# Kernel tuning notes

Hardware: AMD Instinct MI355X
Metric: run time of the kernel (lower is better)

Reference implementation:

```python
import jax, jax.numpy as jnp
import numpy as np

B = 128        # graphs
NPG = 64       # nodes per graph (num_node)
N = B * NPG    # total nodes = 8192
IN = 16        # in_channels
D = 128        # d_model
OUT = 64       # out_channels
CAT = IN * NPG + NPG * NPG  # 5120
EPS = 1e-5


def _lin_init(k, fi, fo):
    s = 1.0 / np.sqrt(fi)
    kw, kb = jax.random.split(k)
    W = jax.random.uniform(kw, (fi, fo), jnp.float32, -s, s)
    b = jax.random.uniform(kb, (fo,), jnp.float32, -s, s)
    return W, b


def setup_inputs() -> dict:
    key = jax.random.key(0)
    ks = jax.random.split(key, 10)
    x = jax.random.normal(ks[0], (N, IN), jnp.float32)
    # complete graph (all i->j pairs, incl. self loops) per graph, offset per graph
    ii = np.repeat(np.arange(NPG), NPG)
    jj = np.tile(np.arange(NPG), NPG)
    off = (np.arange(B) * NPG)[:, None]
    row = (ii[None, :] + off).reshape(-1)
    col = (jj[None, :] + off).reshape(-1)
    edge_index = jnp.asarray(np.stack([row, col]), jnp.int32)  # [2, E]
    E = edge_index.shape[1]
    edge_weight = jax.random.uniform(ks[1], (E,), jnp.float32)
    batch = jnp.repeat(jnp.arange(B, dtype=jnp.int32), NPG)
    W1, b1 = _lin_init(ks[2], IN, D)
    W2, b2 = _lin_init(ks[3], D, D)
    Wm0, bm0 = _lin_init(ks[4], D + CAT, D)
    Wm1, bm1 = _lin_init(ks[5], D, D)
    Wm2, bm2 = _lin_init(ks[6], D, D)
    Wout, bout = _lin_init(ks[7], D, OUT)
    ones = jnp.ones((D,), jnp.float32)
    zeros = jnp.zeros((D,), jnp.float32)
    return dict(x=x, edge_index=edge_index, edge_weight=edge_weight, batch=batch,
                W1=W1, b1=b1, W2=W2, b2=b2,
                Wm0=Wm0, bm0=bm0, g0=ones, be0=zeros,
                Wm1=Wm1, bm1=bm1, g1=ones, be1=zeros,
                Wm2=Wm2, bm2=bm2, g2=ones, be2=zeros,
                Wout=Wout, bout=bout)


def _gcn_conv(h_in, row, col, ew, W, b):
    # PyG GCNConv: linear first, then D^-1/2 (A) D^-1/2 aggregation (self loops already present)
    h = h_in @ W                                             # [N, F]
    deg = jax.ops.segment_sum(ew, col, num_segments=N)       # in-degree by edge weight
    dinv = jnp.where(deg > 0, jax.lax.rsqrt(deg), 0.0)
    norm = dinv[row] * ew * dinv[col]                        # [E]
    out = jax.ops.segment_sum(norm[:, None] * h[row], col, num_segments=N)
    return out + b


def _bn(h, g, b):
    # BatchNorm1d, training-mode math (biased variance), eps=1e-5
    m = jnp.mean(h, axis=0)
    v = jnp.var(h, axis=0)
    return g * (h - m) * jax.lax.rsqrt(v + EPS) + b


def reference(x, edge_index, edge_weight, batch,
              W1, b1, W2, b2,
              Wm0, bm0, g0, be0,
              Wm1, bm1, g1, be1,
              Wm2, bm2, g2, be2,
              Wout, bout):
    row, col = edge_index[0], edge_index[1]
    h = _gcn_conv(x, row, col, edge_weight, W1, b1)
    h = jax.nn.relu(h)
    h = _gcn_conv(h, row, col, edge_weight, W2, b2)
    # global_mean_pool
    sums = jax.ops.segment_sum(h, batch, num_segments=B)
    cnt = jax.ops.segment_sum(jnp.ones((N,), h.dtype), batch, num_segments=B)
    pooled = sums / cnt[:, None]
    pooled = jax.nn.relu(pooled)
    feat = jnp.concatenate([pooled, x.reshape(B, -1), edge_weight.reshape(B, -1)], axis=1)
    feat = jax.nn.relu(feat)
    h = _bn(jax.nn.relu(feat @ Wm0 + bm0), g0, be0)
    h = _bn(jax.nn.relu(h @ Wm1 + bm1), g1, be1)
    h = _bn(jax.nn.relu(h @ Wm2 + bm2), g2, be2)
    return h @ Wout + bout
```

## Files before the change

### kernel.cpp

```cpp
#include <hip/hip_runtime.h>

#define NG 128
#define NPG 64
#define IN 16
#define DM 128
#define NOUT 64
#define EPG 4096
#define NGEMM 160
#define BN_EPS 1e-5f

__global__ __launch_bounds__(256) void k_front(
    const float* __restrict__ x, const float* __restrict__ ew,
    const float* __restrict__ W1, const float* __restrict__ b1,
    const float* __restrict__ Wm0,
    float* __restrict__ z, float* __restrict__ part, float* __restrict__ stats)
{
    __shared__ __align__(16) float u[15616];
    const int b = blockIdx.x, t = threadIdx.x;

    if (b < 128) {
        float* ew_s   = u;
        float* x_s    = u + 4096;
        float* W1_s   = u + 5120;
        float* P_s    = u + 7168;
        float* b1_s   = u + 15360;
        float* dinv_s = u + 15488;
        float* t_s    = u + 15552;
        float* zp     = u + 4096;
        const int g = b;
        if (b == 0) {
            for (int i = t; i < 768; i += 256) stats[i] = 0.f;
        }
        {
            const float4* ew4 = (const float4*)(ew + g * EPG);
            float4* ews4 = (float4*)ew_s;
            #pragma unroll
            for (int i = 0; i < 4; i++) ews4[t + 256 * i] = ew4[t + 256 * i];
            const int xi = t & 63, k4 = (t >> 6) * 4;
            float4 xv = *(const float4*)(x + g * NPG * IN + xi * IN + k4);
            x_s[(k4 + 0) * 64 + xi] = xv.x;
            x_s[(k4 + 1) * 64 + xi] = xv.y;
            x_s[(k4 + 2) * 64 + xi] = xv.z;
            x_s[(k4 + 3) * 64 + xi] = xv.w;
            ((float4*)W1_s)[t]       = ((const float4*)W1)[t];
            ((float4*)W1_s)[t + 256] = ((const float4*)W1)[t + 256];
            if (t < 128) b1_s[t] = b1[t];
        }
        __syncthreads();

        if (t < NPG) {
            float s = 0.f;
            #pragma unroll 8
            for (int i = 0; i < NPG; i++) s += ew_s[i * NPG + t];
            dinv_s[t] = (s > 0.f) ? rsqrtf(s) : 0.f;
        }
        __syncthreads();

        {
            const int j = t & 63, q = t >> 6;
            const float dj = dinv_s[j];
            for (int i = q * 16; i < q * 16 + 16; i++) {
                float vv = ew_s[i * NPG + j] * dj;
                #pragma unroll
                for (int off = 32; off > 0; off >>= 1) vv += __shfl_down(vv, off, 64);
                if (j == 0) t_s[i] = dinv_s[i] * vv * (1.f / 64.f);
            }
        }
        __syncthreads();

        {
            const int it = t & 15, ft = t >> 4;
            const int i0 = it * 4, f0 = ft * 8;
            float accp[4][8];
            #pragma unroll
            for (int a = 0; a < 4; a++)
                #pragma unroll
                for (int c = 0; c < 8; c++) accp[a][c] = 0.f;
            #pragma unroll
            for (int k = 0; k < IN; k++) {
                const float4 a4  = *(const float4*)(x_s + k * 64 + i0);
                const float4 b0v = *(const float4*)(W1_s + k * DM + f0);
                const float4 b1v = *(const float4*)(W1_s + k * DM + f0 + 4);
                const float av[4] = {a4.x, a4.y, a4.z, a4.w};
                const float bv[8] = {b0v.x, b0v.y, b0v.z, b0v.w, b1v.x, b1v.y, b1v.z, b1v.w};
                #pragma unroll
                for (int a = 0; a < 4; a++)
                    #pragma unroll
                    for (int c = 0; c < 8; c++) accp[a][c] += av[a] * bv[c];
            }
            #pragma unroll
            for (int a = 0; a < 4; a++) {
                float4* o = (float4*)(P_s + (i0 + a) * DM + f0);
                o[0] = make_float4(accp[a][0], accp[a][1], accp[a][2], accp[a][3]);
                o[1] = make_float4(accp[a][4], accp[a][5], accp[a][6], accp[a][7]);
            }
        }
        __syncthreads();

        for (int i = t; i < EPG; i += 256) ew_s[i] *= dinv_s[i >> 6];
        __syncthreads();

        {
            const int jt = t & 15, ft = t >> 4;
            const int j0 = jt * 4, f0 = ft * 8;
            float acc[4][8];
            #pragma unroll
            for (int a = 0; a < 4; a++)
                #pragma unroll
                for (int c = 0; c < 8; c++) acc[a][c] = 0.f;
            #pragma unroll 4
            for (int k = 0; k < 64; k++) {
                const float4 a4  = *(const float4*)(ew_s + k * 64 + j0);
                const float4 b0v = *(const float4*)(P_s + k * DM + f0);
                const float4 b1v = *(const float4*)(P_s + k * DM + f0 + 4);
                const float av[4] = {a4.x, a4.y, a4.z, a4.w};
                const float bv[8] = {b0v.x, b0v.y, b0v.z, b0v.w, b1v.x, b1v.y, b1v.z, b1v.w};
                #pragma unroll
                for (int a = 0; a < 4; a++)
                    #pragma unroll
                    for (int c = 0; c < 8; c++) acc[a][c] += av[a] * bv[c];
            }
            float zpart[8];
            #pragma unroll
            for (int c = 0; c < 8; c++) zpart[c] = 0.f;
            #pragma unroll
            for (int a = 0; a < 4; a++) {
                const float dj = dinv_s[j0 + a], tj = t_s[j0 + a];
                #pragma unroll
                for (int c = 0; c < 8; c++) {
                    float h = fmaxf(dj * acc[a][c] + b1_s[f0 + c], 0.f);
                    zpart[c] += tj * h;
                }
            }
            float4* zo = (float4*)(zp + jt * 132 + f0);
            zo[0] = make_float4(zpart[0], zpart[1], zpart[2], zpart[3]);
            zo[1] = make_float4(zpart[4], zpart[5], zpart[6], zpart[7]);
        }
        __syncthreads();

        if (t < 128) {
            float s = 0.f;
            #pragma unroll
            for (int jt = 0; jt < 16; jt++) s += zp[jt * 132 + t];
            z[g * DM + t] = s;
        }
    } else {
        const int c = b - 128;
        const int kc = c >> 1, fh = c & 1;
        float* a_s = u;
        float* b_s = u + 8448;

        const float* src; int stride, off;
        if (kc < 16) { src = x;  stride = 1024; off = kc * 64; }
        else         { src = ew; stride = 4096; off = (kc - 16) * 64; }
        const int K0 = 128 + kc * 64;

        #pragma unroll 4
        for (int it = 0; it < 32; it++) {
            int idx = it * 256 + t;
            int gg = idx >> 6, k = idx & 63;
            a_s[k * 132 + gg] = fmaxf(src[gg * stride + off + k], 0.f);
        }
        #pragma unroll 4
        for (int it = 0; it < 16; it++) {
            int idx = it * 256 + t;
            int k = idx >> 6, fl = idx & 63;
            b_s[k * 64 + fl] = Wm0[(K0 + k) * 128 + fh * 64 + fl];
        }
        __syncthreads();

        const int gthr = t & 31, fthr = t >> 5;
        const int g0 = gthr * 4, f0 = fthr * 8;
        float acc[4][8];
        #pragma unroll
        for (int i = 0; i < 4; i++)
            #pragma unroll
            for (int jx = 0; jx < 8; jx++) acc[i][jx] = 0.f;

        #pragma unroll 4
        for (int k = 0; k < 64; k++) {
            const float4 a4  = *(const float4*)(a_s + k * 132 + g0);
            const float4 c0v = *(const float4*)(b_s + k * 64 + f0);
            const float4 c1v = *(const float4*)(b_s + k * 64 + f0 + 4);
            const float av[4] = {a4.x, a4.y, a4.z, a4.w};
            const float bv[8] = {c0v.x, c0v.y, c0v.z, c0v.w, c1v.x, c1v.y, c1v.z, c1v.w};
            #pragma unroll
            for (int i = 0; i < 4; i++)
                #pragma unroll
                for (int jx = 0; jx < 8; jx++) acc[i][jx] += av[i] * bv[jx];
        }

        float* pp = part + c * 8192;
        #pragma unroll
        for (int i = 0; i < 4; i++) {
            float4* o = (float4*)(pp + (g0 + i) * 64 + f0);
            o[0] = make_float4(acc[i][0], acc[i][1], acc[i][2], acc[i][3]);
            o[1] = make_float4(acc[i][4], acc[i][5], acc[i][6], acc[i][7]);
        }
    }
}

__global__ __launch_bounds__(256) void k_reduce_bn0(
    const float* __restrict__ part, const float* __restrict__ zbuf,
    const float* __restrict__ W2, const float* __restrict__ b2,
    const float* __restrict__ Wm0, const float* __restrict__ bm0,
    float* __restrict__ v0, float* __restrict__ stats0)
{
    __shared__ __align__(16) float W2_s[16384];
    __shared__ __align__(16) float z_s[512];
    __shared__ float Wm0s[2048];
    __shared__ float pooled_s[4 * 130];
    __shared__ float pps[64];
    __shared__ float r1[256];
    __shared__ float sv[64], sv2[64];

    const int bx = blockIdx.x, t = threadIdx.x;
    const int fgrp = bx & 7, gt = bx >> 3;
    const int fsub = t & 15, gl = (t >> 4) & 3, ch = t >> 6;
    const int f = fgrp * 16 + fsub, g = gt * 4 + gl;
    const int fh = f >> 6, fl = f & 63;

    const float* p = part + (size_t)(2 * (ch * 20) + fh) * 8192 + g * 64 + fl;
    float v = 0.f;
    #pragma unroll 5
    for (int cc = 0; cc < 20; cc++) v += p[(size_t)cc * 2 * 8192];

    {
        const float4* w24 = (const float4*)W2;
        float4* w2s4 = (float4*)W2_s;
        #pragma unroll
        for (int i = 0; i < 16; i++) w2s4[t + 256 * i] = w24[t + 256 * i];
        if (t < 128) ((float4*)z_s)[t] = ((const float4*)(zbuf + gt * 512))[t];
        for (int idx = t; idx < 2048; idx += 256) {
            int k = idx >> 4, fs = idx & 15;
            Wm0s[idx] = Wm0[k * DM + fgrp * 16 + fs];
        }
    }
    r1[t] = v;
    __syncthreads();

    {
        const int gp = t >> 6, k0 = t & 63;
        float a0 = 0.f, a1 = 0.f;
        #pragma unroll 4
        for (int m = 0; m < DM; m++) {
            const float zm = z_s[gp * DM + m];
            a0 += zm * W2_s[m * DM + k0];
            a1 += zm * W2_s[m * DM + k0 + 64];
        }
        pooled_s[gp * 130 + k0]      = fmaxf(a0 + b2[k0], 0.f);
        pooled_s[gp * 130 + k0 + 64] = fmaxf(a1 + b2[k0 + 64], 0.f);
    }
    __syncthreads();
    if (t < 64) {
        const int gl2 = t >> 4, fs = t & 15;
        float a = 0.f;
        #pragma unroll 8
        for (int k = 0; k < DM; k++) a += pooled_s[gl2 * 130 + k] * Wm0s[k * 16 + fs];
        pps[t] = a;
    }
    __syncthreads();
    if (ch == 0) {
        v = r1[t] + r1[t + 64] + r1[t + 128] + r1[t + 192] + bm0[f] + pps[t];
        v = fmaxf(v, 0.f);
        v0[g * DM + f] = v;
        sv[t] = v; sv2[t] = v * v;
    }
    __syncthreads();
    if (t < 16) {
        float s1 = sv[t] + sv[t + 16] + sv[t + 32] + sv[t + 48];
        float s2 = sv2[t] + sv2[t + 16] + sv2[t + 32] + sv2[t + 48];
        atomicAdd(&stats0[(fgrp * 16 + t) * 2], s1);
        atomicAdd(&stats0[(fgrp * 16 + t) * 2 + 1], s2);
    }
}

__global__ __launch_bounds__(256) void k_mlp(
    const float* __restrict__ vin, const float* __restrict__ statsin,
    const float* __restrict__ gbn, const float* __restrict__ bbn,
    const float* __restrict__ W, const float* __restrict__ bias,
    float* __restrict__ vout, float* __restrict__ statsout)
{
    __shared__ float h_s[128 * 129];
    __shared__ float wcol[128];
    __shared__ float scale_s[128], shift_s[128];
    __shared__ float pc[128];
    __shared__ float rr[4];
    const int f = blockIdx.x, t = threadIdx.x;
    if (t < 128) {
        float s1 = statsin[t * 2], s2 = statsin[t * 2 + 1];
        float m = s1 * (1.f / 128.f);
        float var = s2 * (1.f / 128.f) - m * m;
        float sc = gbn[t] * rsqrtf(var + BN_EPS);
        scale_s[t] = sc;
        shift_s[t] = bbn[t] - m * sc;
        wcol[t] = W[t * 128 + f];
    }
    __syncthreads();
    #pragma unroll 4
    for (int it = 0; it < 16; it++) {
        int idx = it * 256 + t;
        int g = idx >> 5, k4 = (idx & 31) * 4;
        float4 vv = ((const float4*)vin)[idx];
        float* hp = h_s + g * 129 + k4;
        hp[0] = vv.x * scale_s[k4 + 0] + shift_s[k4 + 0];
        hp[1] = vv.y * scale_s[k4 + 1] + shift_s[k4 + 1];
        hp[2] = vv.z * scale_s[k4 + 2] + shift_s[k4 + 2];
        hp[3] = vv.w * scale_s[k4 + 3] + shift_s[k4 + 3];
    }
    __syncthreads();
    const int g = t & 127, kh = t >> 7;
    float acc = 0.f;
    #pragma unroll 8
    for (int k = kh * 64; k < kh * 64 + 64; k++) acc += h_s[g * 129 + k] * wcol[k];
    if (kh) pc[g] = acc;
    __syncthreads();
    if (t < 128) {
        float v = fmaxf(acc + pc[t] + bias[f], 0.f);
        vout[t * 128 + f] = v;
        float s1 = v, s2 = v * v;
        #pragma unroll
        for (int off = 32; off > 0; off >>= 1) {
            s1 += __shfl_down(s1, off, 64);
            s2 += __shfl_down(s2, off, 64);
        }
        if ((t & 63) == 0) { rr[(t >> 6) * 2] = s1; rr[(t >> 6) * 2 + 1] = s2; }
    }
    __syncthreads();
    if (t == 0) {
        statsout[f * 2]     = rr[0] + rr[2];
        statsout[f * 2 + 1] = rr[1] + rr[3];
    }
}

__global__ __launch_bounds__(128) void k_out(
    const float* __restrict__ vin, const float* __restrict__ statsin,
    const float* __restrict__ gbn, const float* __restrict__ bbn,
    const float* __restrict__ Wo, const float* __restrict__ bo,
    float* __restrict__ out)
{
    __shared__ __align__(16) float Wo_s[128 * 64];
    __shared__ float vrow[2][128];
    __shared__ float scale_s[128], shift_s[128];
    const int b = blockIdx.x, t = threadIdx.x, g0 = b * 2;
    {
        float s1 = statsin[t * 2], s2 = statsin[t * 2 + 1];
        float m = s1 * (1.f / 128.f);
        float var = s2 * (1.f / 128.f) - m * m;
        float sc = gbn[t] * rsqrtf(var + BN_EPS);
        scale_s[t] = sc;
        shift_s[t] = bbn[t] - m * sc;
    }
    __syncthreads();
    {
        const float4* wo4 = (const float4*)Wo;
        float4* wos4 = (float4*)Wo_s;
        #pragma unroll
        for (int it = 0; it < 16; it++) wos4[it * 128 + t] = wo4[it * 128 + t];
    }
    if (t < 64) {
        int g2 = t >> 5, k4 = (t & 31) * 4;
        float4 vv = ((const float4*)(vin + g0 * 128))[t];
        vrow[g2][k4 + 0] = vv.x * scale_s[k4 + 0] + shift_s[k4 + 0];
        vrow[g2][k4 + 1] = vv.y * scale_s[k4 + 1] + shift_s[k4 + 1];
        vrow[g2][k4 + 2] = vv.z * scale_s[k4 + 2] + shift_s[k4 + 2];
        vrow[g2][k4 + 3] = vv.w * scale_s[k4 + 3] + shift_s[k4 + 3];
    }
    __syncthreads();
    const int g2 = t >> 6, o = t & 63;
    float acc = bo[o];
    #pragma unroll 8
    for (int k = 0; k < 128; k++) acc += vrow[g2][k] * Wo_s[k * 64 + o];
    out[(g0 + g2) * NOUT + o] = acc;
}

extern "C" void kernel_launch(void* const* d_in, const int* in_sizes, int n_in,
                              void* d_out, int out_size, void* d_ws, size_t ws_size,
                              hipStream_t stream)
{
    const float* x   = (const float*)d_in[0];
    const float* ew  = (const float*)d_in[2];
    const float* W1  = (const float*)d_in[4];
    const float* b1  = (const float*)d_in[5];
    const float* W2  = (const float*)d_in[6];
    const float* b2  = (const float*)d_in[7];
    const float* Wm0 = (const float*)d_in[8];
    const float* bm0 = (const float*)d_in[9];
    const float* g0  = (const float*)d_in[10];
    const float* be0 = (const float*)d_in[11];
    const float* Wm1 = (const float*)d_in[12];
    const float* bm1 = (const float*)d_in[13];
    const float* g1  = (const float*)d_in[14];
    const float* be1 = (const float*)d_in[15];
    const float* Wm2 = (const float*)d_in[16];
    const float* bm2 = (const float*)d_in[17];
    const float* g2  = (const float*)d_in[18];
    const float* be2 = (const float*)d_in[19];
    const float* Wo  = (const float*)d_in[20];
    const float* bo  = (const float*)d_in[21];

    float* ws     = (float*)d_ws;
    float* zbuf   = ws;
    float* part   = zbuf + 16384;
    float* v0     = part + NGEMM * 8192;
    float* v1     = v0 + 16384;
    float* v2     = v1 + 16384;
    float* stats  = v2 + 16384;

    k_front<<<128 + NGEMM, 256, 0, stream>>>(x, ew, W1, b1, Wm0, zbuf, part, stats);
    k_reduce_bn0<<<256, 256, 0, stream>>>(part, zbuf, W2, b2, Wm0, bm0, v0, stats);
    k_mlp<<<128, 256, 0, stream>>>(v0, stats,       g0, be0, Wm1, bm1, v1, stats + 256);
    k_mlp<<<128, 256, 0, stream>>>(v1, stats + 256, g1, be1, Wm2, bm2, v2, stats + 512);
    k_out<<<NOUT, 128, 0, stream>>>(v2, stats + 512, g2, be2, Wo, bo, (float*)d_out);
}
```

Before: 136.9 us.

## Move pooled W2/Wm0 projections into front kernel, rebalance split-K, split MLP blocks

Each graph block in the front kernel now computes pooled = relu(z@W2+b2) and its Wm0 contribution itself. This removes the per-block reload of the full 64KB W2 and the Wm0 slice in the reduce kernel. The split-K GEMM over the concatenated features now uses 64 chunks of 80 columns (256 blocks total) in place of 80 chunks of 64, so the reduce reads fewer partials. The MLP layers launch 256 blocks, each covering half the graphs, and accumulate BN stats through atomics. The trade-off is more serial work in the graph blocks, a longer K loop per GEMM block and extra atomic traffic.

```diff
diff --git a/kernel.cpp b/kernel.cpp
--- a/kernel.cpp
+++ b/kernel.cpp
@@ -6,29 +6,34 @@
 #define DM 128
 #define NOUT 64
 #define EPG 4096
-#define NGEMM 160
+#define NCH 128
 #define BN_EPS 1e-5f
 
 __global__ __launch_bounds__(256) void k_front(
     const float* __restrict__ x, const float* __restrict__ ew,
     const float* __restrict__ W1, const float* __restrict__ b1,
+    const float* __restrict__ W2, const float* __restrict__ b2,
     const float* __restrict__ Wm0,
-    float* __restrict__ z, float* __restrict__ part, float* __restrict__ stats)
+    float* __restrict__ part, float* __restrict__ ppart,
+    float* __restrict__ stats)
 {
-    __shared__ __align__(16) float u[15616];
-    const int b = blockIdx.x, t = threadIdx.x;
-
-    if (b < 128) {
-        float* ew_s   = u;
-        float* x_s    = u + 4096;
-        float* W1_s   = u + 5120;
-        float* P_s    = u + 7168;
-        float* b1_s   = u + 15360;
-        float* dinv_s = u + 15488;
-        float* t_s    = u + 15552;
-        float* zp     = u + 4096;
-        const int g = b;
-        if (b == 0) {
+    __shared__ __align__(16) float u[16128];
+    const int bid = blockIdx.x, t = threadIdx.x;
+
+    if (bid < 128) {
+        float* ew_s     = u;
+        float* x_s      = u + 4096;
+        float* W1_s     = u + 5120;
+        float* P_s      = u + 7168;
+        float* b1_s     = u + 15360;
+        float* dinv_s   = u + 15488;
+        float* t_s      = u + 15552;
+        float* zp       = u + 4096;
+        float* z_full   = u + 15616;
+        float* pooled_s = u + 15744;
+        float* pp2      = u + 15872;
+        const int g = bid;
+        if (bid == 0) {
             for (int i = t; i < 768; i += 256) stats[i] = 0.f;
         }
         {
@@ -142,30 +147,60 @@
             float s = 0.f;
             #pragma unroll
             for (int jt = 0; jt < 16; jt++) s += zp[jt * 132 + t];
-            z[g * DM + t] = s;
-        }
+            z_full[t] = s;
+        }
+        __syncthreads();
+
+        {
+            const int c = t & 127, kh = t >> 7;
+            float acc = 0.f;
+            #pragma unroll 8
+            for (int k = kh * 64; k < kh * 64 + 64; k++)
+                acc += z_full[k] * W2[k * DM + c];
+            pp2[kh * 128 + c] = acc;
+        }
+        __syncthreads();
+        if (t < 128) pooled_s[t] = fmaxf(pp2[t] + pp2[128 + t] + b2[t], 0.f);
+        __syncthreads();
+
+        {
+            const int f = t & 127, kh = t >> 7;
+            float acc = 0.f;
+            #pragma unroll 8
+            for (int k = kh * 64; k < kh * 64 + 64; k++)
+                acc += pooled_s[k] * Wm0[k * DM + f];
+            pp2[kh * 128 + f] = acc;
+        }
+        __syncthreads();
+        if (t < 128) ppart[g * DM + t] = pp2[t] + pp2[128 + t];
     } else {
-        const int c = b - 128;
+        const int c = bid - 128;
         const int kc = c >> 1, fh = c & 1;
+        const int K0 = kc * 80;
         float* a_s = u;
-        float* b_s = u + 8448;
-
-        const float* src; int stride, off;
-        if (kc < 16) { src = x;  stride = 1024; off = kc * 64; }
-        else         { src = ew; stride = 4096; off = (kc - 16) * 64; }
-        const int K0 = 128 + kc * 64;
+        float* b_s = u + 10560;
 
         #pragma unroll 4
         for (int it = 0; it < 32; it++) {
             int idx = it * 256 + t;
             int gg = idx >> 6, k = idx & 63;
-            a_s[k * 132 + gg] = fmaxf(src[gg * stride + off + k], 0.f);
+            int K = K0 + k;
+            float val = (K < 1024) ? x[gg * 1024 + K] : ew[gg * 4096 + (K - 1024)];
+            a_s[k * 132 + gg] = fmaxf(val, 0.f);
         }
         #pragma unroll 4
-        for (int it = 0; it < 16; it++) {
+        for (int it = 0; it < 8; it++) {
+            int idx = it * 256 + t;
+            int gg = idx >> 4, k = 64 + (idx & 15);
+            int K = K0 + k;
+            float val = (K < 1024) ? x[gg * 1024 + K] : ew[gg * 4096 + (K - 1024)];
+            a_s[k * 132 + gg] = fmaxf(val, 0.f);
+        }
+        #pragma unroll 4
+        for (int it = 0; it < 20; it++) {
             int idx = it * 256 + t;
             int k = idx >> 6, fl = idx & 63;
-            b_s[k * 64 + fl] = Wm0[(K0 + k) * 128 + fh * 64 + fl];
+            b_s[k * 64 + fl] = Wm0[(128 + K0 + k) * 128 + fh * 64 + fl];
         }
         __syncthreads();
 
@@ -178,7 +213,7 @@
             for (int jx = 0; jx < 8; jx++) acc[i][jx] = 0.f;
 
         #pragma unroll 4
-        for (int k = 0; k < 64; k++) {
+        for (int k = 0; k < 80; k++) {
             const float4 a4  = *(const float4*)(a_s + k * 132 + g0);
             const float4 c0v = *(const float4*)(b_s + k * 64 + f0);
             const float4 c1v = *(const float4*)(b_s + k * 64 + f0 + 4);
@@ -190,7 +225,7 @@
                 for (int jx = 0; jx < 8; jx++) acc[i][jx] += av[i] * bv[jx];
         }
 
-        float* pp = part + c * 8192;
+        float* pp = part + (size_t)c * 8192;
         #pragma unroll
         for (int i = 0; i < 4; i++) {
             float4* o = (float4*)(pp + (g0 + i) * 64 + f0);
@@ -201,67 +236,28 @@
 }
 
 __global__ __launch_bounds__(256) void k_reduce_bn0(
-    const float* __restrict__ part, const float* __restrict__ zbuf,
-    const float* __restrict__ W2, const float* __restrict__ b2,
-    const float* __restrict__ Wm0, const float* __restrict__ bm0,
-    float* __restrict__ v0, float* __restrict__ stats0)
+    const float* __restrict__ part, const float* __restrict__ ppart,
+    const float* __restrict__ bm0, float* __restrict__ v0,
+    float* __restrict__ stats0)
 {
-    __shared__ __align__(16) float W2_s[16384];
-    __shared__ __align__(16) float z_s[512];
-    __shared__ float Wm0s[2048];
-    __shared__ float pooled_s[4 * 130];
-    __shared__ float pps[64];
     __shared__ float r1[256];
     __shared__ float sv[64], sv2[64];
-
     const int bx = blockIdx.x, t = threadIdx.x;
     const int fgrp = bx & 7, gt = bx >> 3;
     const int fsub = t & 15, gl = (t >> 4) & 3, ch = t >> 6;
     const int f = fgrp * 16 + fsub, g = gt * 4 + gl;
     const int fh = f >> 6, fl = f & 63;
 
-    const float* p = part + (size_t)(2 * (ch * 20) + fh) * 8192 + g * 64 + fl;
+    const float* p = part + (size_t)(2 * (ch * 16) + fh) * 8192 + g * 64 + fl;
     float v = 0.f;
-    #pragma unroll 5
-    for (int cc = 0; cc < 20; cc++) v += p[(size_t)cc * 2 * 8192];
-
-    {
-        const float4* w24 = (const float4*)W2;
-        float4* w2s4 = (float4*)W2_s;
-        #pragma unroll
-        for (int i = 0; i < 16; i++) w2s4[t + 256 * i] = w24[t + 256 * i];
-        if (t < 128) ((float4*)z_s)[t] = ((const float4*)(zbuf + gt * 512))[t];
-        for (int idx = t; idx < 2048; idx += 256) {
-            int k = idx >> 4, fs = idx & 15;
-            Wm0s[idx] = Wm0[k * DM + fgrp * 16 + fs];
-        }
-    }
+    #pragma unroll 4
+    for (int cc = 0; cc < 16; cc++) v += p[(size_t)cc * 16384];
+
     r1[t] = v;
     __syncthreads();
-
-    {
-        const int gp = t >> 6, k0 = t & 63;
-        float a0 = 0.f, a1 = 0.f;
-        #pragma unroll 4
-        for (int m = 0; m < DM; m++) {
-            const float zm = z_s[gp * DM + m];
-            a0 += zm * W2_s[m * DM + k0];
-            a1 += zm * W2_s[m * DM + k0 + 64];
-        }
-        pooled_s[gp * 130 + k0]      = fmaxf(a0 + b2[k0], 0.f);
-        pooled_s[gp * 130 + k0 + 64] = fmaxf(a1 + b2[k0 + 64], 0.f);
-    }
-    __syncthreads();
-    if (t < 64) {
-        const int gl2 = t >> 4, fs = t & 15;
-        float a = 0.f;
-        #pragma unroll 8
-        for (int k = 0; k < DM; k++) a += pooled_s[gl2 * 130 + k] * Wm0s[k * 16 + fs];
-        pps[t] = a;
-    }
-    __syncthreads();
     if (ch == 0) {
-        v = r1[t] + r1[t + 64] + r1[t + 128] + r1[t + 192] + bm0[f] + pps[t];
+        v = r1[t] + r1[t + 64] + r1[t + 128] + r1[t + 192]
+          + bm0[f] + ppart[g * DM + f];
         v = fmaxf(v, 0.f);
         v0[g * DM + f] = v;
         sv[t] = v; sv2[t] = v * v;
@@ -281,12 +277,12 @@
     const float* __restrict__ W, const float* __restrict__ bias,
     float* __restrict__ vout, float* __restrict__ statsout)
 {
-    __shared__ float h_s[128 * 129];
+    __shared__ float scale_s[128], shift_s[128];
     __shared__ float wcol[128];
-    __shared__ float scale_s[128], shift_s[128];
-    __shared__ float pc[128];
-    __shared__ float rr[4];
-    const int f = blockIdx.x, t = threadIdx.x;
+    __shared__ float pc[256];
+    __shared__ float h_s[64 * 129];
+    const int b = blockIdx.x, t = threadIdx.x;
+    const int f = b & 127, gh = b >> 7;
     if (t < 128) {
         float s1 = statsin[t * 2], s2 = statsin[t * 2 + 1];
         float m = s1 * (1.f / 128.f);
@@ -297,39 +293,42 @@
         wcol[t] = W[t * 128 + f];
     }
     __syncthreads();
-    #pragma unroll 4
-    for (int it = 0; it < 16; it++) {
+    const int g0r = gh * 64;
+    const float4* vin4 = (const float4*)(vin + g0r * 128);
+    #pragma unroll
+    for (int it = 0; it < 8; ++it) {
         int idx = it * 256 + t;
-        int g = idx >> 5, k4 = (idx & 31) * 4;
-        float4 vv = ((const float4*)vin)[idx];
-        float* hp = h_s + g * 129 + k4;
+        int gl = idx >> 5, k4 = (idx & 31) * 4;
+        float4 vv = vin4[idx];
+        float* hp = h_s + gl * 129 + k4;
         hp[0] = vv.x * scale_s[k4 + 0] + shift_s[k4 + 0];
         hp[1] = vv.y * scale_s[k4 + 1] + shift_s[k4 + 1];
         hp[2] = vv.z * scale_s[k4 + 2] + shift_s[k4 + 2];
         hp[3] = vv.w * scale_s[k4 + 3] + shift_s[k4 + 3];
     }
     __syncthreads();
-    const int g = t & 127, kh = t >> 7;
-    float acc = 0.f;
-    #pragma unroll 8
-    for (int k = kh * 64; k < kh * 64 + 64; k++) acc += h_s[g * 129 + k] * wcol[k];
-    if (kh) pc[g] = acc;
-    __syncthreads();
-    if (t < 128) {
-        float v = fmaxf(acc + pc[t] + bias[f], 0.f);
-        vout[t * 128 + f] = v;
+    {
+        const int gl = t & 63, kh = t >> 6;
+        float acc = 0.f;
+        #pragma unroll 8
+        for (int k = kh * 32; k < kh * 32 + 32; ++k) acc += h_s[gl * 129 + k] * wcol[k];
+        pc[gl * 4 + kh] = acc;
+    }
+    __syncthreads();
+    if (t < 64) {
+        float v = fmaxf(pc[t * 4] + pc[t * 4 + 1] + pc[t * 4 + 2] + pc[t * 4 + 3]
+                        + bias[f], 0.f);
+        vout[(size_t)(g0r + t) * 128 + f] = v;
         float s1 = v, s2 = v * v;
         #pragma unroll
         for (int off = 32; off > 0; off >>= 1) {
             s1 += __shfl_down(s1, off, 64);
             s2 += __shfl_down(s2, off, 64);
         }
-        if ((t & 63) == 0) { rr[(t >> 6) * 2] = s1; rr[(t >> 6) * 2 + 1] = s2; }
-    }
-    __syncthreads();
-    if (t == 0) {
-        statsout[f * 2]     = rr[0] + rr[2];
-        statsout[f * 2 + 1] = rr[1] + rr[3];
+        if (t == 0) {
+            atomicAdd(&statsout[f * 2], s1);
+            atomicAdd(&statsout[f * 2 + 1], s2);
+        }
     }
 }
 
@@ -400,16 +399,16 @@
     const float* bo  = (const float*)d_in[21];
 
     float* ws     = (float*)d_ws;
-    float* zbuf   = ws;
-    float* part   = zbuf + 16384;
-    float* v0     = part + NGEMM * 8192;
+    float* part   = ws;
+    float* ppartb = part + NCH * 8192;
+    float* v0     = ppartb + 16384;
     float* v1     = v0 + 16384;
     float* v2     = v1 + 16384;
     float* stats  = v2 + 16384;
 
-    k_front<<<128 + NGEMM, 256, 0, stream>>>(x, ew, W1, b1, Wm0, zbuf, part, stats);
-    k_reduce_bn0<<<256, 256, 0, stream>>>(part, zbuf, W2, b2, Wm0, bm0, v0, stats);
-    k_mlp<<<128, 256, 0, stream>>>(v0, stats,       g0, be0, Wm1, bm1, v1, stats + 256);
-    k_mlp<<<128, 256, 0, stream>>>(v1, stats + 256, g1, be1, Wm2, bm2, v2, stats + 512);
+    k_front<<<256, 256, 0, stream>>>(x, ew, W1, b1, W2, b2, Wm0, part, ppartb, stats);
+    k_reduce_bn0<<<256, 256, 0, stream>>>(part, ppartb, bm0, v0, stats);
+    k_mlp<<<256, 256, 0, stream>>>(v0, stats,       g0, be0, Wm1, bm1, v1, stats + 256);
+    k_mlp<<<256, 256, 0, stream>>>(v1, stats + 256, g1, be1, Wm2, bm2, v2, stats + 512);
     k_out<<<NOUT, 128, 0, stream>>>(v2, stats + 512, g2, be2, Wo, bo, (float*)d_out);
 }
```

Result: no change. 136.0 us (-0.7%).
